# Kernel tuning notes

Hardware: AMD Instinct MI355X
Metric: run time of the kernel (lower is better)

## Reference

```python
import jax, jax.numpy as jnp
import numpy as np

N_FFT = 512
HOP = 128
WIN_LENGTH = 512  # == n_fft, so no window padding needed


def hann_periodic(n):
    # torch.hann_window default is periodic=True
    return (0.5 - 0.5 * jnp.cos(2.0 * jnp.pi * jnp.arange(n) / n)).astype(jnp.float32)


def setup_inputs() -> dict:
    key = jax.random.key(0)
    k1, _ = jax.random.split(key)
    B, C, F, T = 16, 2, N_FFT // 2 + 1, 2048
    X = jax.random.normal(k1, (B, C, F, T, 2), dtype=jnp.float32)
    window = hann_periodic(WIN_LENGTH)
    return {"X": X, "window": window}


def istft(X, window):
    # X: (B, C, F, T, 2) real+imag; onesided, center=True, normalized=False
    Xc = jax.lax.complex(X[..., 0], X[..., 1])          # (B, C, F, T)
    frames = jnp.fft.irfft(Xc, n=N_FFT, axis=-2)        # (B, C, n_fft, T)
    frames = frames * window[None, None, :, None]       # windowed frames
    frames = jnp.moveaxis(frames, -2, -1)               # (B, C, T, n_fft)

    T = frames.shape[-2]
    full_len = N_FFT + (T - 1) * HOP
    # overlap-add scatter indices: (T, n_fft)
    idx = (jnp.arange(T) * HOP)[:, None] + jnp.arange(N_FFT)[None, :]

    y = jnp.zeros(frames.shape[:2] + (full_len,), frames.dtype).at[..., idx].add(frames)
    # window-envelope normalization (sum of squared windows, overlap-added)
    env = jnp.zeros((full_len,), window.dtype).at[idx].add(
        jnp.broadcast_to(window * window, (T, N_FFT)))

    pad = N_FFT // 2  # center=True trims n_fft//2 from both ends
    return y[..., pad:full_len - pad] / env[pad:full_len - pad]


def reference(X, window):
    return istft(X, window)  # (B, C, (T-1)*hop)
```

## Files before the change

### kernel.cpp

```cpp
#include <hip/hip_runtime.h>
#include <hip/hip_bf16.h>

#define NFFT    512
#define HOPSZ   128
#define FBINS   257
#define TFR     2048
#define NBC     32
#define OUTLEN  262016
#define SPAD    256

typedef __bf16 bf16x8 __attribute__((ext_vector_type(8)));
typedef float  f32x4  __attribute__((ext_vector_type(4)));

static __device__ __forceinline__ float bf2f(unsigned short u) {
    union { unsigned int i; float f; } x; x.i = (unsigned int)u << 16; return x.f;
}

__device__ __forceinline__ void gld_lds16(const void* g, void* l) {
    __builtin_amdgcn_global_load_lds(
        (const __attribute__((address_space(1))) unsigned int*)g,
        (__attribute__((address_space(3))) unsigned int*)l, 16, 0, 0);
}

__global__ __launch_bounds__(256) void k_wgen(const float* __restrict__ wnd,
                                              uint4* __restrict__ Wf) {
    const int gid  = blockIdx.x * 256 + threadIdx.x;
    const int lane = gid & 63;
    const int rt   = (gid >> 6) & 31;
    const int ks   = gid >> 11;
    const int n    = rt * 16 + (lane & 15);
    const int kb   = ks * 32 + ((lane >> 4) << 2);
    const float wn = wnd[n] * (1.0f / 512.0f);
    union { uint4 u; unsigned short h[8]; } o;
    #pragma unroll
    for (int j = 0; j < 8; ++j) {
        const int k = kb + (j & 3) + 16 * (j >> 2);
        float val = 0.0f;
        if (k < 2 * FBINS) {
            const int f = k >> 1;
            const bool edge = (f == 0) || (f == 256);
            const float cf = edge ? 1.0f : 2.0f;
            const int m = (f * n) & (NFFT - 1);
            const float ang = (float)m * 0.01227184630308513f;
            float s, c;
            __sincosf(ang, &s, &c);
            val = (k & 1) ? (edge ? 0.0f : -cf * wn * s) : (cf * wn * c);
        }
        __hip_bfloat16 hb = __float2bfloat16(val);
        o.h[j] = *(unsigned short*)&hb;
    }
    Wf[gid] = o.u;
}

__global__ __launch_bounds__(256, 4) void k_mm(
    const float* __restrict__ X,
    const uint4* __restrict__ Wf,
    __hip_bfloat16* __restrict__ frames)
{
    __shared__ uint4  Ab[1024];
    __shared__ float2 Bf[16][64];

    const int tid  = threadIdx.x;
    const int lane = tid & 63;
    const int w    = tid >> 6;
    const int q    = lane >> 4;
    const int rlo  = lane & 15;

    const int bid = blockIdx.x;
    const int id  = (bid & 7) * 256 + (bid >> 3);
    const int m     = id & 1;
    const int panel = (id >> 1) & 31;
    const int bc    = id >> 6;
    const int t0b   = panel << 6;

    const float2* __restrict__ X2 = (const float2*)X + (size_t)bc * FBINS * TFR;

    const int br = tid >> 5;
    const int bck = tid & 31;

    f32x4 acc[4][4] = {};

    for (int ks = 0; ks < 16; ++ks) {
        __syncthreads();
        const uint4* asrc = Wf + (size_t)ks * 2048 + m * 1024;
        #pragma unroll
        for (int r = 0; r < 4; ++r)
            gld_lds16(asrc + r * 256 + tid, &Ab[r * 256 + tid]);
        {
            const float2* b0 = X2 + (size_t)(ks * 16 + br) * TFR + t0b + 2 * bck;
            gld_lds16(b0,                    &Bf[br][2 * bck]);
            gld_lds16(b0 + (size_t)8 * TFR,  &Bf[br + 8][2 * bck]);
        }
        __syncthreads();
        uint4 a[4], b[4];
        #pragma unroll
        for (int ni = 0; ni < 4; ++ni) {
            const float2* Bp = &Bf[2 * q][ni * 16 + rlo];
            float2 v0 = Bp[0];
            float2 v1 = Bp[64];
            float2 v2 = Bp[8 * 64];
            float2 v3 = Bp[9 * 64];
            union { unsigned short h[8]; uint4 u; } pk;
            __hip_bfloat16 t;
            t = __float2bfloat16(v0.x); pk.h[0] = *(unsigned short*)&t;
            t = __float2bfloat16(v0.y); pk.h[1] = *(unsigned short*)&t;
            t = __float2bfloat16(v1.x); pk.h[2] = *(unsigned short*)&t;
            t = __float2bfloat16(v1.y); pk.h[3] = *(unsigned short*)&t;
            t = __float2bfloat16(v2.x); pk.h[4] = *(unsigned short*)&t;
            t = __float2bfloat16(v2.y); pk.h[5] = *(unsigned short*)&t;
            t = __float2bfloat16(v3.x); pk.h[6] = *(unsigned short*)&t;
            t = __float2bfloat16(v3.y); pk.h[7] = *(unsigned short*)&t;
            b[ni] = pk.u;
        }
        #pragma unroll
        for (int mi = 0; mi < 4; ++mi) a[mi] = Ab[(4 * w + mi) * 64 + lane];
        #pragma unroll
        for (int mi = 0; mi < 4; ++mi)
            #pragma unroll
            for (int ni = 0; ni < 4; ++ni)
                acc[mi][ni] = __builtin_amdgcn_mfma_f32_16x16x32_bf16(
                    __builtin_bit_cast(bf16x8, a[mi]),
                    __builtin_bit_cast(bf16x8, b[ni]), acc[mi][ni], 0, 0, 0);
    }

    unsigned short* fb = (unsigned short*)frames;
    #pragma unroll
    for (int mi = 0; mi < 4; ++mi) {
        const int nbase = m * 256 + (w << 6) + (mi << 4) + (q << 2);
        #pragma unroll
        for (int ni = 0; ni < 4; ++ni) {
            const int t = t0b + ni * 16 + rlo;
            union { ushort4 u; __hip_bfloat16 hh[4]; } pk;
            pk.hh[0] = __float2bfloat16(acc[mi][ni][0]);
            pk.hh[1] = __float2bfloat16(acc[mi][ni][1]);
            pk.hh[2] = __float2bfloat16(acc[mi][ni][2]);
            pk.hh[3] = __float2bfloat16(acc[mi][ni][3]);
            *(ushort4*)(fb + (((size_t)(bc * TFR + t)) << 9) + nbase) = pk.u;
        }
    }
}

__global__ __launch_bounds__(256) void k_ola(
    const __hip_bfloat16* __restrict__ frames,
    const float* __restrict__ wnd,
    const float* __restrict__ X,
    float* __restrict__ out)
{
    const int bc = blockIdx.y;
    const int o  = (blockIdx.x * 256 + threadIdx.x) * 4;
    if (o >= OUTLEN) return;
    const int s   = o + SPAD;
    const int tb_ = s >> 7;
    const int nb  = s & (HOPSZ - 1);
    const unsigned short* fb = (const unsigned short*)frames + (size_t)bc * TFR * NFFT;
    const float* Xre = X + (((size_t)bc * FBINS + 256) * TFR) * 2;
    const float sA = ((nb & 1) ? -1.0f : 1.0f) * (1.0f / 512.0f);
    float y0 = 0.f, y1 = 0.f, y2 = 0.f, y3 = 0.f;
    float e0 = 0.f, e1 = 0.f, e2 = 0.f, e3 = 0.f;
    #pragma unroll
    for (int r = 0; r < 4; ++r) {
        const int t = tb_ - r;
        if ((unsigned)t > (unsigned)(TFR - 1)) continue;
        const int n = nb + (r << 7);
        ushort4 v = *(const ushort4*)(fb + (size_t)t * NFFT + n);
        float4  wv = *(const float4*)(wnd + n);
        const float c = sA * Xre[2 * t];
        y0 += bf2f(v.x) + c * wv.x; e0 += wv.x * wv.x;
        y1 += bf2f(v.y) - c * wv.y; e1 += wv.y * wv.y;
        y2 += bf2f(v.z) + c * wv.z; e2 += wv.z * wv.z;
        y3 += bf2f(v.w) - c * wv.w; e3 += wv.w * wv.w;
    }
    float4 res = make_float4(y0 / e0, y1 / e1, y2 / e2, y3 / e3);
    *(float4*)(out + (size_t)bc * OUTLEN + o) = res;
}

extern "C" void kernel_launch(void* const* d_in, const int* in_sizes, int n_in,
                              void* d_out, int out_size, void* d_ws, size_t ws_size,
                              hipStream_t stream) {
    (void)in_sizes; (void)n_in; (void)out_size; (void)ws_size;
    const float* X   = (const float*)d_in[0];
    const float* wnd = (const float*)d_in[1];
    float* out = (float*)d_out;

    uint4* Wf = (uint4*)d_ws;
    __hip_bfloat16* frames = (__hip_bfloat16*)((char*)d_ws + (1 << 20));

    k_wgen<<<136, 256, 0, stream>>>(wnd, Wf);
    k_mm<<<2048, 256, 0, stream>>>(X, Wf, frames);
    k_ola<<<dim3((OUTLEN / 4 + 255) / 256, NBC), 256, 0, stream>>>(frames, wnd, X, out);
}
```

Baseline: 81.65 us.

## Load DFT weights directly to registers with double-buffered prefetch in GEMM

The A operand (windowed DFT basis) is now read from global memory straight into registers instead of being staged through LDS. The next k-slice is prefetched into a second register set while the current one is used, and the k loop is fully unrolled in pairs. This removes the LDS traffic for A and overlaps its global latency with the MFMA work. The cost is higher register pressure, which is why the launch bound drops from 4 to 3 waves' worth of occupancy, and each B stage still needs two barriers.

```diff
diff --git a/kernel.cpp b/kernel.cpp
--- a/kernel.cpp
+++ b/kernel.cpp
@@ -52,12 +52,11 @@
     Wf[gid] = o.u;
 }
 
-__global__ __launch_bounds__(256, 4) void k_mm(
+__global__ __launch_bounds__(256, 3) void k_mm(
     const float* __restrict__ X,
     const uint4* __restrict__ Wf,
     __hip_bfloat16* __restrict__ frames)
 {
-    __shared__ uint4  Ab[1024];
     __shared__ float2 Bf[16][64];
 
     const int tid  = threadIdx.x;
@@ -75,24 +74,26 @@
 
     const float2* __restrict__ X2 = (const float2*)X + (size_t)bc * FBINS * TFR;
 
-    const int br = tid >> 5;
+    const int br  = tid >> 5;
     const int bck = tid & 31;
 
     f32x4 acc[4][4] = {};
-
-    for (int ks = 0; ks < 16; ++ks) {
-        __syncthreads();
-        const uint4* asrc = Wf + (size_t)ks * 2048 + m * 1024;
-        #pragma unroll
-        for (int r = 0; r < 4; ++r)
-            gld_lds16(asrc + r * 256 + tid, &Ab[r * 256 + tid]);
-        {
-            const float2* b0 = X2 + (size_t)(ks * 16 + br) * TFR + t0b + 2 * bck;
-            gld_lds16(b0,                    &Bf[br][2 * bck]);
-            gld_lds16(b0 + (size_t)8 * TFR,  &Bf[br + 8][2 * bck]);
-        }
-        __syncthreads();
-        uint4 a[4], b[4];
+    uint4 arA[4], arB[4];
+
+    auto loadA = [&](int ks, uint4 (&ar)[4]) {
+        const uint4* ap = Wf + (size_t)ks * 2048 + m * 1024 + (4 * w) * 64 + lane;
+        ar[0] = ap[0];
+        ar[1] = ap[64];
+        ar[2] = ap[128];
+        ar[3] = ap[192];
+    };
+    auto stageB = [&](int ks) {
+        const float2* b0 = X2 + (size_t)(ks * 16 + br) * TFR + t0b + 2 * bck;
+        gld_lds16(b0,                   &Bf[br][2 * bck]);
+        gld_lds16(b0 + (size_t)8 * TFR, &Bf[br + 8][2 * bck]);
+    };
+    auto computeP = [&](uint4 (&ar)[4]) {
+        uint4 b[4];
         #pragma unroll
         for (int ni = 0; ni < 4; ++ni) {
             const float2* Bp = &Bf[2 * q][ni * 16 + rlo];
@@ -113,14 +114,27 @@
             b[ni] = pk.u;
         }
         #pragma unroll
-        for (int mi = 0; mi < 4; ++mi) a[mi] = Ab[(4 * w + mi) * 64 + lane];
-        #pragma unroll
         for (int mi = 0; mi < 4; ++mi)
             #pragma unroll
             for (int ni = 0; ni < 4; ++ni)
                 acc[mi][ni] = __builtin_amdgcn_mfma_f32_16x16x32_bf16(
-                    __builtin_bit_cast(bf16x8, a[mi]),
+                    __builtin_bit_cast(bf16x8, ar[mi]),
                     __builtin_bit_cast(bf16x8, b[ni]), acc[mi][ni], 0, 0, 0);
+    };
+
+    loadA(0, arA);
+    #pragma unroll
+    for (int kp = 0; kp < 8; ++kp) {
+        __syncthreads();
+        stageB(2 * kp);
+        loadA(2 * kp + 1, arB);
+        __syncthreads();
+        computeP(arA);
+        __syncthreads();
+        stageB(2 * kp + 1);
+        if (kp < 7) loadA(2 * kp + 2, arA);
+        __syncthreads();
+        computeP(arB);
     }
 
     unsigned short* fb = (unsigned short*)frames;
```

Measured after the change: 83.06 us. About the same (+1.7%).
